# Optimization experiments

Measured on AMD Instinct MI355X. Metric: run time of the kernel, lower is better.

## Reference

```python
import jax, jax.numpy as jnp
import numpy as np

B_BLK = 64      # sparse_block_size
LOCAL = 4       # sparse_local_num_blocks
GLOB = 2        # sparse_global_num_blocks
STRIDE = 4      # sparse_global_block_stride
NH = 16
NKV = 4
HD = 128
SCALE = HD ** -0.5
NEG = -1e9


def _build_block_index(num_blocks):
    """Static per-query-block key-block index table + validity mask."""
    max_sel = LOCAL + 1 + GLOB
    idx = np.zeros((num_blocks, max_sel), np.int32)
    valid = np.zeros((num_blocks, max_sel), bool)
    for t in range(num_blocks):
        local = list(range(max(0, t - LOCAL), t + 1))
        cand = list(range(0, t + 1, max(1, STRIDE)))
        glob = cand[-GLOB:] if (GLOB > 0 and len(cand) > 0) else []
        sel = sorted(set(local + glob))
        idx[t, :len(sel)] = sel
        valid[t, :len(sel)] = True
    return idx, valid


def _rotate_half(x):
    x1, x2 = jnp.split(x, 2, axis=-1)
    return jnp.concatenate((-x2, x1), axis=-1)


def setup_inputs() -> dict:
    key = jax.random.key(0)
    ks = jax.random.split(key, 7)
    bsz, S, H = 1, 4096, 2048
    return {
        "hidden_states": jax.random.normal(ks[0], (bsz, S, H), jnp.float32) * 0.02,
        "cos": jax.random.uniform(ks[1], (bsz, S, HD), jnp.float32, -1.0, 1.0),
        "sin": jax.random.uniform(ks[2], (bsz, S, HD), jnp.float32, -1.0, 1.0),
        "wq": jax.random.normal(ks[3], (NH * HD, H), jnp.float32) * 0.02,
        "wk": jax.random.normal(ks[4], (NKV * HD, H), jnp.float32) * 0.02,
        "wv": jax.random.normal(ks[5], (NKV * HD, H), jnp.float32) * 0.02,
        "wo": jax.random.normal(ks[6], (H, NH * HD), jnp.float32) * 0.02,
    }


def reference(hidden_states, cos, sin, wq, wk, wv, wo):
    b, S, H = hidden_states.shape
    # QKV projections (nn.Linear: x @ W.T), split heads -> [b, h, S, d]
    q = (hidden_states @ wq.T).reshape(b, S, NH, HD).transpose(0, 2, 1, 3)
    k = (hidden_states @ wk.T).reshape(b, S, NKV, HD).transpose(0, 2, 1, 3)
    v = (hidden_states @ wv.T).reshape(b, S, NKV, HD).transpose(0, 2, 1, 3)
    # RoPE (cos/sin broadcast over heads)
    c = cos[:, None, :, :]
    s = sin[:, None, :, :]
    q = q * c + _rotate_half(q) * s
    k = k * c + _rotate_half(k) * s
    # GQA: repeat KV heads
    n_rep = NH // NKV
    k = jnp.repeat(k, n_rep, axis=1)
    v = jnp.repeat(v, n_rep, axis=1)
    # Block-sparse local+global attention (S divisible by B_BLK -> no padding)
    T = S // B_BLK
    q_blk = q.reshape(b, NH, T, B_BLK, HD)
    k_blk = k.reshape(b, NH, T, B_BLK, HD)
    v_blk = v.reshape(b, NH, T, B_BLK, HD)
    idx, valid = _build_block_index(T)           # [T, Smax] static
    Smax = idx.shape[1]
    k_sel = k_blk[:, :, idx]                     # [b,h,T,Smax,Bk,d]
    v_sel = v_blk[:, :, idx]
    scores = jnp.einsum('bhtqd,bhtspd->bhtqsp', q_blk, k_sel) * SCALE
    # causal intra-block mask on the diagonal block, -inf on padded slots
    intra = jnp.triu(jnp.full((B_BLK, B_BLK), NEG, jnp.float32), 1)
    is_diag = jnp.asarray(idx == np.arange(T)[:, None], jnp.float32)  # [T,Smax]
    mask = is_diag[:, None, :, None] * intra[None, :, None, :]        # [T,Bq,Smax,Bk]
    mask = mask + jnp.where(jnp.asarray(valid)[:, None, :, None], 0.0, NEG)
    scores = scores + mask[None, None]
    scores = scores.reshape(b, NH, T, B_BLK, Smax * B_BLK)
    probs = jax.nn.softmax(scores, axis=-1)
    out = jnp.einsum('bhtqk,bhtkd->bhtqd', probs,
                     v_sel.reshape(b, NH, T, Smax * B_BLK, HD))
    out = out.reshape(b, NH, S, HD).transpose(0, 2, 1, 3).reshape(b, S, NH * HD)
    return out @ wo.T
```

## Files before the change

### kernel.cpp

```cpp
#include <hip/hip_runtime.h>

typedef unsigned short u16;
typedef short bf16x8 __attribute__((ext_vector_type(8)));
typedef float f32x4 __attribute__((ext_vector_type(4)));

#define S_LEN 4096
#define NHEADS 16
#define NKVH 4
#define HDIM 128
#define HID 2048
#define NQKV 3072

__device__ __forceinline__ u16 f2bf(float x) {
  union { float f; unsigned u; } v; v.f = x;
  unsigned r = v.u + 0x7fffu + ((v.u >> 16) & 1u);
  return (u16)(r >> 16);
}
__device__ __forceinline__ float bf2f(u16 x) {
  union { unsigned u; float f; } v; v.u = ((unsigned)x) << 16;
  return v.f;
}
__device__ __forceinline__ void async16(u16* lds, const u16* g) {
  __builtin_amdgcn_global_load_lds((const __attribute__((address_space(1))) void*)g,
                                   (__attribute__((address_space(3))) void*)lds, 16, 0, 0);
}

__global__ __launch_bounds__(256) void cast_all(const float* __restrict__ hs,
                                                const float* __restrict__ wq,
                                                const float* __restrict__ wk,
                                                const float* __restrict__ wv,
                                                const float* __restrict__ wo,
                                                u16* __restrict__ ws) {
  int i = blockIdx.x * 256 + threadIdx.x;
  const float* src; int si;
  if (i < 2097152)      { src = hs; si = i; }
  else if (i < 3145728) { src = wq; si = i - 2097152; }
  else if (i < 3407872) { src = wk; si = i - 3145728; }
  else if (i < 3670016) { src = wv; si = i - 3407872; }
  else                  { src = wo; si = i - 3670016; }
  float4 v = ((const float4*)src)[si];
  ushort4 o;
  o.x = f2bf(v.x); o.y = f2bf(v.y); o.z = f2bf(v.z); o.w = f2bf(v.w);
  ((ushort4*)ws)[i] = o;
}

template<bool OUT_BF16>
__global__ __launch_bounds__(256) void gemm_bt(const u16* __restrict__ A, const u16* __restrict__ B,
                                               void* __restrict__ Cp, int M, int N, int K) {
  __shared__ __align__(16) u16 As[128 * 64];
  __shared__ __align__(16) u16 Bs[128 * 64];
  const int tid = threadIdx.x;
  const int w = tid >> 6, l = tid & 63;
  const int quad = l >> 4, l16 = l & 15;
  const int bm = blockIdx.x, bn = blockIdx.y;
  const int wr = w & 1, wc = w >> 1;

  const size_t abase = (size_t)bm * 128 * K;
  const size_t bbase = (size_t)bn * 128 * K;

  f32x4 acc[4][4];
  for (int i = 0; i < 4; ++i)
    for (int j = 0; j < 4; ++j) acc[i][j] = f32x4{0.f, 0.f, 0.f, 0.f};

  int sm[4], sc[4];
  for (int j = 0; j < 4; ++j) {
    int slot = (w * 4 + j) * 64 + l;
    sm[j] = slot >> 3;
    sc[j] = (slot & 7) ^ (sm[j] & 7);
  }
  int aoff[2][4], boff[2][4];
  for (int ksi = 0; ksi < 2; ++ksi) {
    int cb = ksi * 4 + quad;
    for (int mt = 0; mt < 4; ++mt) {
      int m = wr * 64 + mt * 16 + l16;
      aoff[ksi][mt] = (m * 8 + (cb ^ (m & 7))) * 8;
      int n = wc * 64 + mt * 16 + l16;
      boff[ksi][mt] = (n * 8 + (cb ^ (n & 7))) * 8;
    }
  }

  for (int kt = 0; kt < K; kt += 64) {
    __syncthreads();
    for (int j = 0; j < 4; ++j) {
      async16(&As[(w * 4 + j) * 64 * 8], A + abase + (size_t)sm[j] * K + kt + sc[j] * 8);
      async16(&Bs[(w * 4 + j) * 64 * 8], B + bbase + (size_t)sm[j] * K + kt + sc[j] * 8);
    }
    __syncthreads();
    for (int ksi = 0; ksi < 2; ++ksi) {
      bf16x8 af[4], bv[4];
      for (int mt = 0; mt < 4; ++mt) {
        af[mt] = *(const bf16x8*)&As[aoff[ksi][mt]];
        bv[mt] = *(const bf16x8*)&Bs[boff[ksi][mt]];
      }
      for (int mt = 0; mt < 4; ++mt)
        for (int nt = 0; nt < 4; ++nt)
          acc[mt][nt] = __builtin_amdgcn_mfma_f32_16x16x32_bf16(af[mt], bv[nt], acc[mt][nt], 0, 0, 0);
    }
  }

  const int row_base = bm * 128 + wr * 64;
  const int col_base = bn * 128 + wc * 64;
  for (int mt = 0; mt < 4; ++mt)
    for (int nt = 0; nt < 4; ++nt) {
      int col = col_base + nt * 16 + l16;
      for (int r = 0; r < 4; ++r) {
        int row = row_base + mt * 16 + quad * 4 + r;
        float v = acc[mt][nt][r];
        if (OUT_BF16) ((u16*)Cp)[(size_t)row * N + col] = f2bf(v);
        else          ((float*)Cp)[(size_t)row * N + col] = v;
      }
    }
}

__global__ __launch_bounds__(256) void rope_vtrans(const u16* __restrict__ qkv,
                                                   const float* __restrict__ cosp,
                                                   const float* __restrict__ sinp,
                                                   u16* __restrict__ Q, u16* __restrict__ Kd,
                                                   u16* __restrict__ Vt) {
  __shared__ u16 tile[64][65];
  const int bid = blockIdx.x;
  const int tid = threadIdx.x;
  if (bid < 2560) {
    const float SCALE = 0.08838834764831845f;
    int idx = bid * 256 + tid;
    int d8 = (idx & 7) * 8;
    int hh = (idx >> 3) % 20;
    int s = idx / 160;
    size_t base = (size_t)s * NQKV + hh * 128;

    ushort4 xa = *(const ushort4*)&qkv[base + d8];
    ushort4 xb = *(const ushort4*)&qkv[base + d8 + 4];
    ushort4 ya = *(const ushort4*)&qkv[base + d8 + 64];
    ushort4 yb = *(const ushort4*)&qkv[base + d8 + 68];
    float x[8] = { bf2f(xa.x), bf2f(xa.y), bf2f(xa.z), bf2f(xa.w),
                   bf2f(xb.x), bf2f(xb.y), bf2f(xb.z), bf2f(xb.w) };
    float y[8] = { bf2f(ya.x), bf2f(ya.y), bf2f(ya.z), bf2f(ya.w),
                   bf2f(yb.x), bf2f(yb.y), bf2f(yb.z), bf2f(yb.w) };

    const float* cp = cosp + s * 128 + d8;
    const float* sp = sinp + s * 128 + d8;
    float4 c0 = *(const float4*)(cp);
    float4 c1 = *(const float4*)(cp + 4);
    float4 c2 = *(const float4*)(cp + 64);
    float4 c3 = *(const float4*)(cp + 68);
    float4 s0 = *(const float4*)(sp);
    float4 s1 = *(const float4*)(sp + 4);
    float4 s2 = *(const float4*)(sp + 64);
    float4 s3 = *(const float4*)(sp + 68);
    float cl[8] = { c0.x, c0.y, c0.z, c0.w, c1.x, c1.y, c1.z, c1.w };
    float sl[8] = { s0.x, s0.y, s0.z, s0.w, s1.x, s1.y, s1.z, s1.w };
    float ch[8] = { c2.x, c2.y, c2.z, c2.w, c3.x, c3.y, c3.z, c3.w };
    float sh[8] = { s2.x, s2.y, s2.z, s2.w, s3.x, s3.y, s3.z, s3.w };

    const float g = (hh < NHEADS) ? SCALE : 1.0f;
    u16 o1[8], o2[8];
#pragma unroll
    for (int j = 0; j < 8; ++j) {
      o1[j] = f2bf((x[j] * cl[j] - y[j] * sl[j]) * g);
      o2[j] = f2bf((y[j] * ch[j] + x[j] * sh[j]) * g);
    }
    u16* dst = (hh < NHEADS) ? (Q + ((size_t)hh * S_LEN + s) * HDIM)
                             : (Kd + ((size_t)(hh - NHEADS) * S_LEN + s) * HDIM);
    *(ushort4*)&dst[d8]      = ushort4{o1[0], o1[1], o1[2], o1[3]};
    *(ushort4*)&dst[d8 + 4]  = ushort4{o1[4], o1[5], o1[6], o1[7]};
    *(ushort4*)&dst[d8 + 64] = ushort4{o2[0], o2[1], o2[2], o2[3]};
    *(ushort4*)&dst[d8 + 68] = ushort4{o2[4], o2[5], o2[6], o2[7]};
  } else {
    int vb = bid - 2560;
    int s0 = (vb & 63) * 64;
    int j0 = (vb >> 6) * 64;
    for (int it = 0; it < 16; ++it) {
      int lin = it * 256 + tid;
      int sr = lin >> 6, jc = lin & 63;
      tile[sr][jc] = qkv[(size_t)(s0 + sr) * NQKV + 2560 + j0 + jc];
    }
    __syncthreads();
    for (int it = 0; it < 16; ++it) {
      int lin = it * 256 + tid;
      int dr = lin >> 6, sc = lin & 63;
      Vt[(size_t)(j0 + dr) * S_LEN + s0 + sc] = tile[sc][dr];
    }
  }
}

__global__ __launch_bounds__(256) void attn_kernel(const u16* __restrict__ Q, const u16* __restrict__ K,
                                                   const u16* __restrict__ Vt, u16* __restrict__ Aout) {
  const float NEGF = -30000.0f;
  const int t = blockIdx.x, h = blockIdx.y;
  const int kvh = h >> 2;
  const int tid = threadIdx.x;
  const int w = tid >> 6, l = tid & 63, quad = l >> 4, l16 = l & 15;

  __shared__ __align__(16) u16 Ks[2][64 * 128];
  __shared__ __align__(16) u16 Vs[2][128 * 64];
  __shared__ __align__(16) u16 Ps[4 * 16 * 72];

  int sel[7]; int nsel = 0;
  {
    int g1 = (t >> 2) << 2, g0 = g1 - 4;
    int lo = t - 4; if (lo < 0) lo = 0;
    if (g0 >= 0 && g0 < lo) sel[nsel++] = g0;
    if (g1 < lo) sel[nsel++] = g1;
    for (int b = lo; b <= t; ++b) sel[nsel++] = b;
  }

  const int mq = w * 16 + l16;
  const u16* qptr = Q + ((size_t)h * S_LEN + t * 64 + mq) * HDIM + quad * 8;
  bf16x8 qf[4];
#pragma unroll
  for (int ks = 0; ks < 4; ++ks) qf[ks] = *(const bf16x8*)(qptr + ks * 32);

  const int slot0 = w * 4 * 64 + l;
#define STAGEKV(b, kb) do { \
    const size_t kbase = ((size_t)kvh * S_LEN + (kb) * 64) * HDIM; \
    const size_t vbase = (size_t)kvh * HDIM * S_LEN + (kb) * 64; \
    _Pragma("unroll") \
    for (int j_ = 0; j_ < 4; ++j_) { \
      int slot = slot0 + j_ * 64; \
      int mk = slot >> 4; \
      int ck = (slot & 15) ^ (mk & 15); \
      async16(&Ks[b][(w * 4 + j_) * 64 * 8], K + kbase + mk * 128 + ck * 8); \
      int dv = slot >> 3; \
      int cv = (slot & 7) ^ (dv & 7); \
      async16(&Vs[b][(w * 4 + j_) * 64 * 8], Vt + vbase + (size_t)dv * S_LEN + cv * 8); \
    } } while (0)

  STAGEKV(0, sel[0]);
  __syncthreads();

  float l_run[4];
  for (int r = 0; r < 4; ++r) l_run[r] = 0.f;
  f32x4 oacc[8];
  for (int i = 0; i < 8; ++i) oacc[i] = f32x4{0.f, 0.f, 0.f, 0.f};

  for (int ib = 0; ib < nsel; ++ib) {
    const int kb = sel[ib];
    const int cur = ib & 1;
    if (ib + 1 < nsel) STAGEKV(cur ^ 1, sel[ib + 1]);

    f32x4 sacc[4];
    for (int nt = 0; nt < 4; ++nt) sacc[nt] = f32x4{0.f, 0.f, 0.f, 0.f};
#pragma unroll
    for (int ks = 0; ks < 4; ++ks) {
      int cb = ks * 4 + quad;
#pragma unroll
      for (int nt = 0; nt < 4; ++nt) {
        int n = nt * 16 + l16;
        bf16x8 bv = *(const bf16x8*)&Ks[cur][(n * 16 + (cb ^ (n & 15))) * 8];
        sacc[nt] = __builtin_amdgcn_mfma_f32_16x16x32_bf16(qf[ks], bv, sacc[nt], 0, 0, 0);
      }
    }

    const bool diag = (kb == t);
    for (int r = 0; r < 4; ++r) {
      int qrow = w * 16 + quad * 4 + r;
      float sum = 0.f;
      for (int nt = 0; nt < 4; ++nt) {
        float v = sacc[nt][r];
        if (diag && (nt * 16 + l16) > qrow) v = NEGF;
        float p = __expf(v);
        sum += p;
        Ps[(w * 16 + quad * 4 + r) * 72 + nt * 16 + l16] = f2bf(p);
      }
      for (int off = 1; off < 16; off <<= 1) sum += __shfl_xor(sum, off);
      l_run[r] += sum;
    }

#pragma unroll
    for (int ks = 0; ks < 64; ks += 32) {
      bf16x8 pf = *(const bf16x8*)&Ps[(w * 16 + l16) * 72 + ks + quad * 8];
      int cb = (ks >> 3) + quad;
#pragma unroll
      for (int nt = 0; nt < 8; ++nt) {
        int n = nt * 16 + l16;
        bf16x8 vv = *(const bf16x8*)&Vs[cur][(n * 8 + (cb ^ (n & 7))) * 8];
        oacc[nt] = __builtin_amdgcn_mfma_f32_16x16x32_bf16(pf, vv, oacc[nt], 0, 0, 0);
      }
    }

    __syncthreads();
  }
#undef STAGEKV

  float inv[4];
  for (int r = 0; r < 4; ++r) inv[r] = 1.f / l_run[r];
  const int srow = t * 64 + w * 16 + quad * 4;
  for (int nt = 0; nt < 8; ++nt) {
    int col = h * 128 + nt * 16 + l16;
    for (int r = 0; r < 4; ++r)
      Aout[(size_t)(srow + r) * HID + col] = f2bf(oacc[nt][r] * inv[r]);
  }
}

extern "C" void kernel_launch(void* const* d_in, const int* in_sizes, int n_in,
                              void* d_out, int out_size, void* d_ws, size_t ws_size,
                              hipStream_t stream) {
  const float* hs   = (const float*)d_in[0];
  const float* cosp = (const float*)d_in[1];
  const float* sinp = (const float*)d_in[2];
  const float* wq   = (const float*)d_in[3];
  const float* wk   = (const float*)d_in[4];
  const float* wv   = (const float*)d_in[5];
  const float* wo   = (const float*)d_in[6];

  u16* hsb = (u16*)d_ws;
  u16* W   = hsb + (size_t)S_LEN * HID;
  u16* wob = W + (size_t)NQKV * HID;
  u16* qkv = wob + (size_t)HID * HID;
  u16* Qm  = qkv + (size_t)S_LEN * NQKV;
  u16* Km  = Qm + (size_t)NHEADS * S_LEN * HDIM;
  u16* Vt  = Km + (size_t)NKVH * S_LEN * HDIM;
  u16* att = Vt + (size_t)NKVH * HDIM * S_LEN;

  cast_all<<<18432, 256, 0, stream>>>(hs, wq, wk, wv, wo, (u16*)d_ws);

  gemm_bt<true><<<dim3(32, 24), 256, 0, stream>>>(hsb, W, (void*)qkv, 4096, 3072, 2048);
  rope_vtrans<<<3072, 256, 0, stream>>>(qkv, cosp, sinp, Qm, Km, Vt);
  attn_kernel<<<dim3(64, 16), 256, 0, stream>>>(Qm, Km, Vt, att);
  gemm_bt<false><<<dim3(32, 16), 256, 0, stream>>>(att, wob, d_out, 4096, 2048, 2048);
}
```

Baseline: 263.6 us.

## Process two query blocks per attention workgroup to share staged K/V tiles

Each attention workgroup now handles two adjacent 64-row query blocks, with each wave owning 32 query rows. The workgroup stages the union of the key blocks both query blocks need, and each wave skips key blocks outside its own selection. This halves the grid and reuses each staged K/V tile across more query rows, cutting global-to-LDS traffic. In exchange, each wave holds twice the accumulators and Q fragments, which adds register pressure. Waves also go idle on key blocks their query block does not use.

```diff
diff --git a/kernel.cpp b/kernel.cpp
--- a/kernel.cpp
+++ b/kernel.cpp
@@ -186,29 +186,34 @@
 __global__ __launch_bounds__(256) void attn_kernel(const u16* __restrict__ Q, const u16* __restrict__ K,
                                                    const u16* __restrict__ Vt, u16* __restrict__ Aout) {
   const float NEGF = -30000.0f;
-  const int t = blockIdx.x, h = blockIdx.y;
+  const int tt = blockIdx.x, h = blockIdx.y;
   const int kvh = h >> 2;
   const int tid = threadIdx.x;
   const int w = tid >> 6, l = tid & 63, quad = l >> 4, l16 = l & 15;
+  const int th = tt * 2 + (w >> 1);
+  const int sub = w & 1;
 
   __shared__ __align__(16) u16 Ks[2][64 * 128];
   __shared__ __align__(16) u16 Vs[2][128 * 64];
   __shared__ __align__(16) u16 Ps[4 * 16 * 72];
 
-  int sel[7]; int nsel = 0;
+  const int t1 = 2 * tt + 1;
+  const int g1 = (t1 >> 2) << 2, g0 = g1 - 4;
+  int sel[8]; int nsel = 0;
   {
-    int g1 = (t >> 2) << 2, g0 = g1 - 4;
-    int lo = t - 4; if (lo < 0) lo = 0;
-    if (g0 >= 0 && g0 < lo) sel[nsel++] = g0;
-    if (g1 < lo) sel[nsel++] = g1;
-    for (int b = lo; b <= t; ++b) sel[nsel++] = b;
-  }
-
-  const int mq = w * 16 + l16;
-  const u16* qptr = Q + ((size_t)h * S_LEN + t * 64 + mq) * HDIM + quad * 8;
-  bf16x8 qf[4];
-#pragma unroll
-  for (int ks = 0; ks < 4; ++ks) qf[ks] = *(const bf16x8*)(qptr + ks * 32);
+    int lo_u = 2 * tt - 4; if (lo_u < 0) lo_u = 0;
+    if (g0 >= 0 && g0 < lo_u) sel[nsel++] = g0;
+    for (int b = lo_u; b <= t1; ++b) sel[nsel++] = b;
+  }
+  const int lo_w = (th - 4 < 0) ? 0 : th - 4;
+
+  bf16x8 qf[2][4];
+#pragma unroll
+  for (int mt = 0; mt < 2; ++mt) {
+    const u16* qptr = Q + ((size_t)h * S_LEN + tt * 128 + w * 32 + mt * 16 + l16) * HDIM + quad * 8;
+#pragma unroll
+    for (int ks = 0; ks < 4; ++ks) qf[mt][ks] = *(const bf16x8*)(qptr + ks * 32);
+  }
 
   const int slot0 = w * 4 * 64 + l;
 #define STAGEKV(b, kb) do { \
@@ -228,67 +233,79 @@
   STAGEKV(0, sel[0]);
   __syncthreads();
 
-  float l_run[4];
-  for (int r = 0; r < 4; ++r) l_run[r] = 0.f;
-  f32x4 oacc[8];
-  for (int i = 0; i < 8; ++i) oacc[i] = f32x4{0.f, 0.f, 0.f, 0.f};
+  float l_run[2][4];
+  for (int mt = 0; mt < 2; ++mt)
+    for (int r = 0; r < 4; ++r) l_run[mt][r] = 0.f;
+  f32x4 oacc[2][8];
+  for (int mt = 0; mt < 2; ++mt)
+    for (int i = 0; i < 8; ++i) oacc[mt][i] = f32x4{0.f, 0.f, 0.f, 0.f};
 
   for (int ib = 0; ib < nsel; ++ib) {
     const int kb = sel[ib];
     const int cur = ib & 1;
     if (ib + 1 < nsel) STAGEKV(cur ^ 1, sel[ib + 1]);
 
-    f32x4 sacc[4];
-    for (int nt = 0; nt < 4; ++nt) sacc[nt] = f32x4{0.f, 0.f, 0.f, 0.f};
-#pragma unroll
-    for (int ks = 0; ks < 4; ++ks) {
-      int cb = ks * 4 + quad;
-#pragma unroll
-      for (int nt = 0; nt < 4; ++nt) {
-        int n = nt * 16 + l16;
-        bf16x8 bv = *(const bf16x8*)&Ks[cur][(n * 16 + (cb ^ (n & 15))) * 8];
-        sacc[nt] = __builtin_amdgcn_mfma_f32_16x16x32_bf16(qf[ks], bv, sacc[nt], 0, 0, 0);
+    const bool valid = (kb >= lo_w && kb <= th) || (kb == g0 && g0 >= 0) || (kb == g1);
+    if (valid) {
+      f32x4 sacc[2][4];
+      for (int mt = 0; mt < 2; ++mt)
+        for (int nt = 0; nt < 4; ++nt) sacc[mt][nt] = f32x4{0.f, 0.f, 0.f, 0.f};
+#pragma unroll
+      for (int ks = 0; ks < 4; ++ks) {
+        int cb = ks * 4 + quad;
+#pragma unroll
+        for (int nt = 0; nt < 4; ++nt) {
+          int n = nt * 16 + l16;
+          bf16x8 bv = *(const bf16x8*)&Ks[cur][(n * 16 + (cb ^ (n & 15))) * 8];
+          sacc[0][nt] = __builtin_amdgcn_mfma_f32_16x16x32_bf16(qf[0][ks], bv, sacc[0][nt], 0, 0, 0);
+          sacc[1][nt] = __builtin_amdgcn_mfma_f32_16x16x32_bf16(qf[1][ks], bv, sacc[1][nt], 0, 0, 0);
+        }
       }
-    }
-
-    const bool diag = (kb == t);
-    for (int r = 0; r < 4; ++r) {
-      int qrow = w * 16 + quad * 4 + r;
-      float sum = 0.f;
-      for (int nt = 0; nt < 4; ++nt) {
-        float v = sacc[nt][r];
-        if (diag && (nt * 16 + l16) > qrow) v = NEGF;
-        float p = __expf(v);
-        sum += p;
-        Ps[(w * 16 + quad * 4 + r) * 72 + nt * 16 + l16] = f2bf(p);
+
+      const bool diag = (kb == th);
+#pragma unroll
+      for (int mt = 0; mt < 2; ++mt) {
+        for (int r = 0; r < 4; ++r) {
+          int qrow = sub * 32 + mt * 16 + quad * 4 + r;
+          float sum = 0.f;
+          for (int nt = 0; nt < 4; ++nt) {
+            float v = sacc[mt][nt][r];
+            if (diag && (nt * 16 + l16) > qrow) v = NEGF;
+            float p = __expf(v);
+            sum += p;
+            Ps[(w * 16 + quad * 4 + r) * 72 + nt * 16 + l16] = f2bf(p);
+          }
+          for (int off = 1; off < 16; off <<= 1) sum += __shfl_xor(sum, off);
+          l_run[mt][r] += sum;
+        }
+#pragma unroll
+        for (int ksv = 0; ksv < 64; ksv += 32) {
+          bf16x8 pf = *(const bf16x8*)&Ps[(w * 16 + l16) * 72 + ksv + quad * 8];
+          int cb = (ksv >> 3) + quad;
+#pragma unroll
+          for (int nt = 0; nt < 8; ++nt) {
+            int n = nt * 16 + l16;
+            bf16x8 vv = *(const bf16x8*)&Vs[cur][(n * 8 + (cb ^ (n & 7))) * 8];
+            oacc[mt][nt] = __builtin_amdgcn_mfma_f32_16x16x32_bf16(pf, vv, oacc[mt][nt], 0, 0, 0);
+          }
+        }
       }
-      for (int off = 1; off < 16; off <<= 1) sum += __shfl_xor(sum, off);
-      l_run[r] += sum;
-    }
-
-#pragma unroll
-    for (int ks = 0; ks < 64; ks += 32) {
-      bf16x8 pf = *(const bf16x8*)&Ps[(w * 16 + l16) * 72 + ks + quad * 8];
-      int cb = (ks >> 3) + quad;
-#pragma unroll
-      for (int nt = 0; nt < 8; ++nt) {
-        int n = nt * 16 + l16;
-        bf16x8 vv = *(const bf16x8*)&Vs[cur][(n * 8 + (cb ^ (n & 7))) * 8];
-        oacc[nt] = __builtin_amdgcn_mfma_f32_16x16x32_bf16(pf, vv, oacc[nt], 0, 0, 0);
-      }
     }
 
     __syncthreads();
   }
 #undef STAGEKV
 
-  float inv[4];
-  for (int r = 0; r < 4; ++r) inv[r] = 1.f / l_run[r];
-  const int srow = t * 64 + w * 16 + quad * 4;
-  for (int nt = 0; nt < 8; ++nt) {
-    int col = h * 128 + nt * 16 + l16;
-    for (int r = 0; r < 4; ++r)
-      Aout[(size_t)(srow + r) * HID + col] = f2bf(oacc[nt][r] * inv[r]);
+#pragma unroll
+  for (int mt = 0; mt < 2; ++mt) {
+    float inv[4];
+    for (int r = 0; r < 4; ++r) inv[r] = 1.f / l_run[mt][r];
+    const int srow = tt * 128 + w * 32 + mt * 16 + quad * 4;
+    for (int nt = 0; nt < 8; ++nt) {
+      int col = h * 128 + nt * 16 + l16;
+      for (int r = 0; r < 4; ++r)
+        Aout[(size_t)(srow + r) * HID + col] = f2bf(oacc[mt][nt][r] * inv[r]);
+    }
   }
 }
 
@@ -316,6 +333,6 @@
 
   gemm_bt<true><<<dim3(32, 24), 256, 0, stream>>>(hsb, W, (void*)qkv, 4096, 3072, 2048);
   rope_vtrans<<<3072, 256, 0, stream>>>(qkv, cosp, sinp, Qm, Km, Vt);
-  attn_kernel<<<dim3(64, 16), 256, 0, stream>>>(Qm, Km, Vt, att);
+  attn_kernel<<<dim3(32, 16), 256, 0, stream>>>(Qm, Km, Vt, att);
   gemm_bt<false><<<dim3(32, 16), 256, 0, stream>>>(att, wob, d_out, 4096, 2048, 2048);
 }
```

Result: slower. 271.5 us (+3.0%).
